# Kernel optimization log

Measured on AMD Instinct MI355X. Metric: run time of the kernel, lower is better.

The kernel has to match this reference:

```python
import jax, jax.numpy as jnp
from jax import lax
import numpy as np

B, T, C = 4, 1024, 1024
NH, HS = 16, 64
K, STRIDE = 32, 16
EPS = 1e-5


def _ln(x, w, b):
    m = jnp.mean(x, axis=-1, keepdims=True)
    v = jnp.mean((x - m) ** 2, axis=-1, keepdims=True)
    return (x - m) * lax.rsqrt(v + EPS) * w + b


def setup_inputs() -> dict:
    key = jax.random.key(0)
    ks = jax.random.split(key, 12)
    s = 0.02
    return {
        'x': jax.random.normal(ks[0], (B, T, C), jnp.float32),
        'c_attn_w': jax.random.normal(ks[1], (C, 3 * C), jnp.float32) * s,
        'c_attn_b': jnp.zeros((3 * C,), jnp.float32),
        'c_proj_w': jax.random.normal(ks[2], (C, C), jnp.float32) * s,
        'c_proj_b': jnp.zeros((C,), jnp.float32),
        'conv_w': jax.random.normal(ks[3], (HS, HS, K), jnp.float32) * s,  # OIH
        'conv_b': jnp.zeros((HS,), jnp.float32),
        'comp_ln_w': jnp.ones((HS,), jnp.float32),
        'comp_ln_b': jnp.zeros((HS,), jnp.float32),
        'ln_local_w': jnp.ones((C,), jnp.float32),
        'ln_local_b': jnp.zeros((C,), jnp.float32),
        'gate_w1': jax.random.normal(ks[4], (2 * C, C), jnp.float32) * s,
        'gate_b1': jnp.zeros((C,), jnp.float32),
        'gate_ln_w': jnp.ones((C,), jnp.float32),
        'gate_ln_b': jnp.zeros((C,), jnp.float32),
        'gate_w2': jax.random.normal(ks[5], (C, 2), jnp.float32) * s,
        'gate_b2': jnp.zeros((2,), jnp.float32),
    }


def _compress(h, conv_w, conv_b, comp_ln_w, comp_ln_b):
    # h: [B, nh, T, hs] -> [B, nh, num_blocks, hs]
    b, nh, t, hs = h.shape
    xr = h.transpose(0, 1, 3, 2).reshape(b * nh, hs, t)  # NCH
    co = lax.conv_general_dilated(xr, conv_w, (STRIDE,), 'VALID',
                                  dimension_numbers=('NCH', 'OIH', 'NCH'))
    co = co + conv_b[None, :, None]
    y = co.transpose(0, 2, 1)  # [B*nh, nb, hs]
    y = _ln(y, comp_ln_w, comp_ln_b)
    y = jax.nn.gelu(y, approximate=False)
    return y.reshape(b, nh, -1, hs)


def _attn(q, k, v, mask):
    # q:[B,nh,T,hs] k,v:[B,nh,Tk,hs], mask:[T,Tk] bool (True=keep)
    scale = 1.0 / jnp.sqrt(jnp.asarray(q.shape[-1], q.dtype))
    att = jnp.einsum('bhqd,bhkd->bhqk', q, k) * scale
    att = jnp.where(mask[None, None], att, jnp.finfo(att.dtype).min)
    att = jax.nn.softmax(att, axis=-1)
    return jnp.einsum('bhqk,bhkd->bhqd', att, v)


def reference(x, c_attn_w, c_attn_b, c_proj_w, c_proj_b, conv_w, conv_b,
              comp_ln_w, comp_ln_b, ln_local_w, ln_local_b,
              gate_w1, gate_b1, gate_ln_w, gate_ln_b, gate_w2, gate_b2):
    b, t, c = x.shape
    qkv = x @ c_attn_w + c_attn_b
    q, k, v = jnp.split(qkv, 3, axis=-1)
    q = q.reshape(b, t, NH, HS).transpose(0, 2, 1, 3)
    k = k.reshape(b, t, NH, HS).transpose(0, 2, 1, 3)
    v = v.reshape(b, t, NH, HS).transpose(0, 2, 1, 3)

    k_comp = _compress(k, conv_w, conv_b, comp_ln_w, comp_ln_b)
    v_comp = _compress(v, conv_w, conv_b, comp_ln_w, comp_ln_b)
    nb = k_comp.shape[2]

    # local branch: flash path with is_causal=True skips the window mask -> plain causal
    causal = jnp.tril(jnp.ones((t, t), bool))
    local = _attn(q, k, v, causal)
    local = local.transpose(0, 2, 1, 3).reshape(b, t, c)
    local_norm = _ln(local, ln_local_w, ln_local_b)

    # compressed branch: causal mask of shape [T, num_blocks], diagonal 0
    comp_mask = jnp.tril(jnp.ones((t, nb), bool), k=0)
    comp = _attn(q, k_comp, v_comp, comp_mask)
    comp = comp.transpose(0, 2, 1, 3).reshape(b, t, c)

    # gating from last-token features
    feats = jnp.concatenate([local_norm[:, -1, :], comp[:, -1, :]], axis=-1)  # [B, 2C]
    h = jax.nn.relu(_ln(feats @ gate_w1 + gate_b1, gate_ln_w, gate_ln_b))
    gates = jax.nn.softmax(h @ gate_w2 + gate_b2, axis=-1)  # [B, 2]
    g = gates[:, None, :]  # [B, 1, 2]
    combined = g[..., 0:1] * local_norm + g[..., 1:2] * comp

    return combined @ c_proj_w + c_proj_b
```

## Files before the change

### kernel.cpp

```cpp
#include <hip/hip_runtime.h>

using u16 = unsigned short;
using f32x4 = __attribute__((ext_vector_type(4))) float;
using s16x8 = __attribute__((ext_vector_type(8))) short;
using u16x4 = __attribute__((ext_vector_type(4))) unsigned short;

__device__ __forceinline__ u16 f2bf(float f) {
  unsigned u = __float_as_uint(f);
  return (u16)((u + 0x7FFFu + ((u >> 16) & 1u)) >> 16);
}

__device__ __forceinline__ f32x4 mfma16(s16x8 a, s16x8 b, f32x4 c) {
  return __builtin_amdgcn_mfma_f32_16x16x32_bf16(a, b, c, 0, 0, 0);
}

__device__ __forceinline__ void gld16(const void* g, void* l) {
  __builtin_amdgcn_global_load_lds(
      (const __attribute__((address_space(1))) unsigned int*)g,
      (__attribute__((address_space(3))) unsigned int*)l, 16, 0, 0);
}

__global__ __launch_bounds__(256) void cast_bf16(const float* __restrict__ in,
                                                 u16* __restrict__ out, int n4) {
  int i = blockIdx.x * 256 + threadIdx.x;
  if (i >= n4) return;
  f32x4 v = *(const f32x4*)(in + (size_t)i * 4);
  u16x4 o = {f2bf(v[0]), f2bf(v[1]), f2bf(v[2]), f2bf(v[3])};
  *(u16x4*)(out + (size_t)i * 4) = o;
}

__global__ __launch_bounds__(256) void transpose_cast(const float* __restrict__ in,
                                                      u16* __restrict__ out,
                                                      int R, int C) {
  __shared__ float t[32][33];
  int bx = blockIdx.x, by = blockIdx.y;
  int tx = threadIdx.x & 31, ty = threadIdx.x >> 5;
#pragma unroll
  for (int r = 0; r < 4; r++) {
    int row = by * 32 + ty + r * 8;
    t[ty + r * 8][tx] = in[(size_t)row * C + bx * 32 + tx];
  }
  __syncthreads();
#pragma unroll
  for (int r = 0; r < 4; r++) {
    int orow = bx * 32 + ty + r * 8;
    out[(size_t)orow * R + by * 32 + tx] = f2bf(t[tx][ty + r * 8]);
  }
}

__device__ __forceinline__ void gemm_mainloop(const u16* A, const u16* Bt, int K,
                                              u16* As, u16* Bs, f32x4 acc[4][4]) {
  const int tid = threadIdx.x;
  const int row = tid >> 2, c16 = tid & 3;
  const int lane = tid & 63, wid = tid >> 6;
  const int wm = wid >> 1, wn = wid & 1, lg = lane >> 4, lr = lane & 15;
  const u16* ga = A + (size_t)row * K + c16 * 8;
  const u16* gb = Bt + (size_t)row * K + c16 * 8;
  const size_t rowskip = (size_t)64 * K;
  for (int k0 = 0; k0 < K; k0 += 32) {
    gld16(ga + k0, As + tid * 8);
    gld16(ga + rowskip + k0, As + 2048 + tid * 8);
    gld16(gb + k0, Bs + tid * 8);
    gld16(gb + rowskip + k0, Bs + 2048 + tid * 8);
    __syncthreads();
    s16x8 af[4], bfr[4];
#pragma unroll
    for (int i = 0; i < 4; i++)
      af[i] = *(const s16x8*)(As + (wm * 64 + i * 16 + lr) * 32 + lg * 8);
#pragma unroll
    for (int j = 0; j < 4; j++)
      bfr[j] = *(const s16x8*)(Bs + (wn * 64 + j * 16 + lr) * 32 + lg * 8);
#pragma unroll
    for (int i = 0; i < 4; i++)
#pragma unroll
      for (int j = 0; j < 4; j++) acc[i][j] = mfma16(af[i], bfr[j], acc[i][j]);
    __syncthreads();
  }
}

__global__ __launch_bounds__(256) void gemm_qkv(const u16* __restrict__ A,
                                                const u16* __restrict__ Bt,
                                                const float* __restrict__ bias,
                                                u16* __restrict__ qo, u16* __restrict__ ko,
                                                u16* __restrict__ kTo, u16* __restrict__ vTo) {
  __shared__ u16 As[4096];
  __shared__ u16 Bs[4096];
  int m0 = blockIdx.x * 128, n0 = blockIdx.y * 128;
  f32x4 acc[4][4] = {};
  gemm_mainloop(A + (size_t)m0 * 1024, Bt + (size_t)n0 * 1024, 1024, As, Bs, acc);
  int lane = threadIdx.x & 63, wid = threadIdx.x >> 6;
  int wm = wid >> 1, wn = wid & 1, lg = lane >> 4, lr = lane & 15;
#pragma unroll
  for (int i = 0; i < 4; i++) {
    int mb = m0 + wm * 64 + i * 16 + lg * 4;
    int b = mb >> 10, tb = mb & 1023;
#pragma unroll
    for (int j = 0; j < 4; j++) {
      int n = n0 + wn * 64 + j * 16 + lr;
      float bs = bias[n];
      int sel = n >> 10, hd = n & 1023, h = hd >> 6, d = hd & 63;
      int bh = b * 16 + h;
      u16 u0 = f2bf(acc[i][j][0] + bs), u1 = f2bf(acc[i][j][1] + bs);
      u16 u2 = f2bf(acc[i][j][2] + bs), u3 = f2bf(acc[i][j][3] + bs);
      if (sel == 0) {
        u16* qp = qo + ((size_t)bh << 16) + ((size_t)tb << 6) + d;
        qp[0] = u0; qp[64] = u1; qp[128] = u2; qp[192] = u3;
      } else if (sel == 1) {
        u16* kp = ko + ((size_t)bh << 16) + ((size_t)tb << 6) + d;
        kp[0] = u0; kp[64] = u1; kp[128] = u2; kp[192] = u3;
        u16x4 pk = {u0, u1, u2, u3};
        *(u16x4*)(kTo + ((size_t)(bh * 64 + d) << 10) + tb) = pk;
      } else {
        u16x4 pk = {u0, u1, u2, u3};
        *(u16x4*)(vTo + ((size_t)(bh * 64 + d) << 10) + tb) = pk;
      }
    }
  }
}

__global__ __launch_bounds__(256) void gemm_proj(const u16* __restrict__ A,
                                                 const u16* __restrict__ Bt,
                                                 const float* __restrict__ bias,
                                                 float* __restrict__ out) {
  __shared__ u16 As[4096];
  __shared__ u16 Bs[4096];
  int m0 = blockIdx.x * 128, n0 = blockIdx.y * 128;
  f32x4 acc[4][4] = {};
  gemm_mainloop(A + (size_t)m0 * 1024, Bt + (size_t)n0 * 1024, 1024, As, Bs, acc);
  int lane = threadIdx.x & 63, wid = threadIdx.x >> 6;
  int wm = wid >> 1, wn = wid & 1, lg = lane >> 4, lr = lane & 15;
#pragma unroll
  for (int i = 0; i < 4; i++) {
    int mb = m0 + wm * 64 + i * 16 + lg * 4;
#pragma unroll
    for (int j = 0; j < 4; j++) {
      int n = n0 + wn * 64 + j * 16 + lr;
      float bs = bias[n];
#pragma unroll
      for (int r = 0; r < 4; r++)
        out[(size_t)(mb + r) * 1024 + n] = acc[i][j][r] + bs;
    }
  }
}

__global__ __launch_bounds__(256) void conv_comp(const u16* __restrict__ kT,
                                                 const u16* __restrict__ vT,
                                                 const u16* __restrict__ cw,
                                                 const float* __restrict__ cb,
                                                 const float* __restrict__ lnw,
                                                 const float* __restrict__ lnb,
                                                 u16* __restrict__ kcomp,
                                                 u16* __restrict__ vcompT) {
  int bh = blockIdx.x, sel = blockIdx.y;
  const u16* src = (sel ? vT : kT) + ((size_t)bh << 16);
  int tid = threadIdx.x, wid = tid >> 6, lane = tid & 63, lg = lane >> 4, lr = lane & 15;
  f32x4 acc[4] = {};
  int arow = wid * 16 + lr;
  if (arow > 62) arow = 62;
  const u16* abase = src + (size_t)arow * 16 + lg * 8;
#pragma unroll 4
  for (int ic = 0; ic < 64; ic++) {
    s16x8 a = *(const s16x8*)(abase + ic * 1024);
#pragma unroll
    for (int j = 0; j < 4; j++) {
      s16x8 bfr = *(const s16x8*)(cw + (size_t)(j * 16 + lr) * 2048 + ic * 32 + lg * 8);
      acc[j] = mfma16(a, bfr, acc[j]);
    }
  }
  float lwv[4], lbv[4];
#pragma unroll
  for (int j = 0; j < 4; j++) {
    int oc = j * 16 + lr;
    float cbv = cb[oc];
    acc[j][0] += cbv; acc[j][1] += cbv; acc[j][2] += cbv; acc[j][3] += cbv;
    lwv[j] = lnw[oc]; lbv[j] = lnb[oc];
  }
#pragma unroll
  for (int r = 0; r < 4; r++) {
    float s = acc[0][r] + acc[1][r] + acc[2][r] + acc[3][r];
    float q = acc[0][r] * acc[0][r] + acc[1][r] * acc[1][r] +
              acc[2][r] * acc[2][r] + acc[3][r] * acc[3][r];
#pragma unroll
    for (int off = 1; off < 16; off <<= 1) {
      s += __shfl_xor(s, off);
      q += __shfl_xor(q, off);
    }
    float mean = s * (1.f / 64.f);
    float var = q * (1.f / 64.f) - mean * mean;
    float rstd = rsqrtf(fmaxf(var, 0.f) + 1e-5f);
    int op = wid * 16 + lg * 4 + r;
#pragma unroll
    for (int j = 0; j < 4; j++) {
      float y = (acc[j][r] - mean) * rstd * lwv[j] + lbv[j];
      y = 0.5f * y * (1.0f + erff(y * 0.70710678118f));
      if (op > 62) y = 0.f;
      int oc = j * 16 + lr;
      if (sel == 0) kcomp[((size_t)bh << 12) + (op << 6) + oc] = f2bf(y);
      else          vcompT[((size_t)bh << 12) + (oc << 6) + op] = f2bf(y);
    }
  }
}

__global__ __launch_bounds__(256, 4) void flash64(const u16* __restrict__ qg,
                                                  const u16* __restrict__ kg,
                                                  const u16* __restrict__ vg,
                                                  float* __restrict__ outg,
                                                  int k_bh, int v_bh, int vrow, int kvmax) {
  __shared__ u16 Ks[2][4096];
  __shared__ u16 Pl[4][1152];
  const int tid = threadIdx.x;
  const int w = tid >> 6, lane = tid & 63, lg = lane >> 4, lr = lane & 15;
  const int idx = blockIdx.x;
  const int nqt = gridDim.x >> 6;
  const int xcd = idx & 7, j = idx >> 3;
  const int bh = xcd * 8 + (j & 7);
  const int qt0 = nqt - 1 - (j >> 3);
  const int q0 = qt0 * 64;
  const int qrow = q0 + w * 16 + lr;
  const u16* qb = qg + ((size_t)bh << 16) + (size_t)qrow * 64 + lg * 8;
  s16x8 qf0 = *(const s16x8*)(qb);
  s16x8 qf1 = *(const s16x8*)(qb + 32);
  const u16* kb = kg + (size_t)bh * k_bh;
  const u16* vb = vg + (size_t)bh * v_bh;
  int nt = qt0 + 1;
  int ntk = (kvmax + 63) >> 6;
  if (nt > ntk) nt = ntk;
  u16* Pw = Pl[w];
  f32x4 ot[4] = {};
  float m = -INFINITY, l = 0.f;
  const float SCL = 0.125f * 1.44269504089f;

  auto stageK = [&](int bufi, int kv0) {
#pragma unroll
    for (int rnd = 0; rnd < 2; rnd++) {
      int o = tid * 16 + rnd * 4096;
      int row = o >> 7;
      int sb = (o & 127) ^ ((row & 7) << 4);
      gld16(kb + (size_t)(kv0 + row) * 64 + (sb >> 1), &Ks[bufi][o >> 1]);
    }
  };

  stageK(0, 0);
  int cur = 0;
  for (int t = 0; t < nt; t++) {
    __syncthreads();
    if (t + 1 < nt) stageK(cur ^ 1, (t + 1) * 64);
    const int kv0 = t * 64;
    const u16* Kb = Ks[cur];
    const bool full = (kv0 + 63 <= q0 + w * 16) && (kv0 + 64 <= kvmax);
    s16x8 vlo[4];
#pragma unroll
    for (int d4 = 0; d4 < 4; d4++)
      vlo[d4] = *(const s16x8*)(vb + (size_t)(d4 * 16 + lr) * vrow + kv0 + lg * 8);
    f32x4 st[4];
    __builtin_amdgcn_s_setprio(1);
#pragma unroll
    for (int kvt = 0; kvt < 4; kvt++) {
      int rr = kvt * 16 + lr;
      int sw = (rr & 7) << 4;
      s16x8 k0 = *(const s16x8*)(Kb + (((rr << 7) + ((lg * 16) ^ sw)) >> 1));
      s16x8 k1 = *(const s16x8*)(Kb + (((rr << 7) + ((64 + lg * 16) ^ sw)) >> 1));
      f32x4 z = {};
      z = mfma16(k0, qf0, z);
      z = mfma16(k1, qf1, z);
      st[kvt] = z;
    }
    __builtin_amdgcn_s_setprio(0);
    s16x8 vhi[4];
#pragma unroll
    for (int d4 = 0; d4 < 4; d4++)
      vhi[d4] = *(const s16x8*)(vb + (size_t)(d4 * 16 + lr) * vrow + kv0 + 32 + lg * 8);
    float p[16];
    float tm = -INFINITY;
    if (full) {
#pragma unroll
      for (int kvt = 0; kvt < 4; kvt++)
#pragma unroll
        for (int r = 0; r < 4; r++) {
          float v = st[kvt][r] * SCL;
          p[kvt * 4 + r] = v;
          tm = fmaxf(tm, v);
        }
    } else {
#pragma unroll
      for (int kvt = 0; kvt < 4; kvt++)
#pragma unroll
        for (int r = 0; r < 4; r++) {
          int kvi = kv0 + kvt * 16 + lg * 4 + r;
          float v = st[kvt][r] * SCL;
          v = (kvi <= qrow && kvi < kvmax) ? v : -INFINITY;
          p[kvt * 4 + r] = v;
          tm = fmaxf(tm, v);
        }
    }
    tm = fmaxf(tm, __shfl_xor(tm, 16));
    tm = fmaxf(tm, __shfl_xor(tm, 32));
    if (!__all(tm <= m)) {
      float mnew = fmaxf(m, tm);
      float fac = exp2f(m - mnew);
      l *= fac;
#pragma unroll
      for (int d4 = 0; d4 < 4; d4++) {
        ot[d4][0] *= fac; ot[d4][1] *= fac; ot[d4][2] *= fac; ot[d4][3] *= fac;
      }
      m = mnew;
    }
    float ls = 0.f;
#pragma unroll
    for (int i = 0; i < 16; i++) {
      float e = exp2f(p[i] - m);
      p[i] = e;
      ls += e;
    }
    ls += __shfl_xor(ls, 16);
    ls += __shfl_xor(ls, 32);
    l += ls;
#pragma unroll
    for (int kvt = 0; kvt < 4; kvt++) {
      unsigned w0 = (unsigned)f2bf(p[kvt * 4 + 0]) | ((unsigned)f2bf(p[kvt * 4 + 1]) << 16);
      unsigned w1 = (unsigned)f2bf(p[kvt * 4 + 2]) | ((unsigned)f2bf(p[kvt * 4 + 3]) << 16);
      uint2 pk = {w0, w1};
      *(uint2*)(Pw + lr * 72 + kvt * 16 + lg * 4) = pk;
    }
    s16x8 bp0 = *(const s16x8*)(Pw + lr * 72 + lg * 8);
    s16x8 bp1 = *(const s16x8*)(Pw + lr * 72 + 32 + lg * 8);
    __builtin_amdgcn_s_setprio(1);
#pragma unroll
    for (int d4 = 0; d4 < 4; d4++) {
      ot[d4] = mfma16(vlo[d4], bp0, ot[d4]);
      ot[d4] = mfma16(vhi[d4], bp1, ot[d4]);
    }
    __builtin_amdgcn_s_setprio(0);
    cur ^= 1;
  }
  float inv = 1.f / l;
  int b = bh >> 4, h = bh & 15;
  float* op = outg + ((size_t)((b << 10) + qrow) << 10) + h * 64;
#pragma unroll
  for (int d4 = 0; d4 < 4; d4++) {
    f32x4 v;
#pragma unroll
    for (int c = 0; c < 4; c++) v[c] = ot[d4][c] * inv;
    *(f32x4*)(op + d4 * 16 + lg * 4) = v;
  }
}

__global__ __launch_bounds__(256) void ln_rows(float* __restrict__ x,
                                               const float* __restrict__ w,
                                               const float* __restrict__ b) {
  __shared__ float red[8];
  size_t row = blockIdx.x;
  float* xr = x + (row << 10);
  int tid = threadIdx.x;
  f32x4 v = *(const f32x4*)(xr + tid * 4);
  float s = v[0] + v[1] + v[2] + v[3];
  float q = v[0] * v[0] + v[1] * v[1] + v[2] * v[2] + v[3] * v[3];
#pragma unroll
  for (int off = 32; off >= 1; off >>= 1) {
    s += __shfl_xor(s, off);
    q += __shfl_xor(q, off);
  }
  int wid = tid >> 6;
  if ((tid & 63) == 0) { red[wid * 2] = s; red[wid * 2 + 1] = q; }
  __syncthreads();
  s = red[0] + red[2] + red[4] + red[6];
  q = red[1] + red[3] + red[5] + red[7];
  float mean = s * (1.0f / 1024.0f);
  float var = q * (1.0f / 1024.0f) - mean * mean;
  float rstd = rsqrtf(fmaxf(var, 0.f) + 1e-5f);
  f32x4 wv = *(const f32x4*)(w + tid * 4);
  f32x4 bv = *(const f32x4*)(b + tid * 4);
  f32x4 o;
#pragma unroll
  for (int c = 0; c < 4; c++) o[c] = (v[c] - mean) * rstd * wv[c] + bv[c];
  *(f32x4*)(xr + tid * 4) = o;
}

__global__ __launch_bounds__(256) void gate_partial(const float* __restrict__ ln,
                                                    const float* __restrict__ comp,
                                                    const float* __restrict__ w1,
                                                    float* __restrict__ partial) {
  __shared__ float f[4][32];
  int ib = blockIdx.x, i0 = ib * 32, tid = threadIdx.x;
  if (tid < 128) {
    int bb = tid >> 5, ii = tid & 31;
    int i = i0 + ii;
    const float* src = (i < 1024) ? ln : comp;
    int ic = i & 1023;
    f[bb][ii] = src[((size_t)(bb * 1024 + 1023) << 10) + ic];
  }
  __syncthreads();
  float acc[4][4] = {};
  for (int ii = 0; ii < 32; ii++) {
    float f0 = f[0][ii], f1 = f[1][ii], f2 = f[2][ii], f3 = f[3][ii];
#pragma unroll
    for (int jj = 0; jj < 4; jj++) {
      float w = w1[(size_t)(i0 + ii) * 1024 + jj * 256 + tid];
      acc[jj][0] += f0 * w; acc[jj][1] += f1 * w;
      acc[jj][2] += f2 * w; acc[jj][3] += f3 * w;
    }
  }
#pragma unroll
  for (int jj = 0; jj < 4; jj++)
#pragma unroll
    for (int bb = 0; bb < 4; bb++)
      partial[(size_t)((ib << 2) + bb) * 1024 + jj * 256 + tid] = acc[jj][bb];
}

__global__ __launch_bounds__(1024) void gate_finish(const float* __restrict__ partial,
                                                    const float* __restrict__ b1,
                                                    const float* __restrict__ lnw,
                                                    const float* __restrict__ lnb,
                                                    const float* __restrict__ w2,
                                                    const float* __restrict__ b2,
                                                    float* __restrict__ g) {
  __shared__ float redA[16], redB[16];
  int b = blockIdx.x, j = threadIdx.x;
  float s = b1[j];
#pragma unroll 4
  for (int ib = 0; ib < 64; ib++) s += partial[(size_t)((ib << 2) + b) * 1024 + j];
  float sa = s, sb = s * s;
#pragma unroll
  for (int off = 32; off >= 1; off >>= 1) {
    sa += __shfl_xor(sa, off);
    sb += __shfl_xor(sb, off);
  }
  int wid = j >> 6;
  if ((j & 63) == 0) { redA[wid] = sa; redB[wid] = sb; }
  __syncthreads();
  if (j == 0) {
    float A = 0, Bv = 0;
    for (int k2 = 0; k2 < 16; k2++) { A += redA[k2]; Bv += redB[k2]; }
    redA[0] = A; redB[0] = Bv;
  }
  __syncthreads();
  float S = redA[0], Q = redB[0];
  float mean = S * (1.f / 1024.f), var = Q * (1.f / 1024.f) - mean * mean;
  float rstd = rsqrtf(fmaxf(var, 0.f) + 1e-5f);
  float hn = (s - mean) * rstd * lnw[j] + lnb[j];
  hn = fmaxf(hn, 0.f);
  float c0 = hn * w2[j * 2], c1 = hn * w2[j * 2 + 1];
  __syncthreads();
  float ra = c0, rb = c1;
#pragma unroll
  for (int off = 32; off >= 1; off >>= 1) {
    ra += __shfl_xor(ra, off);
    rb += __shfl_xor(rb, off);
  }
  if ((j & 63) == 0) { redA[wid] = ra; redB[wid] = rb; }
  __syncthreads();
  if (j == 0) {
    float A = 0, Bv = 0;
    for (int k2 = 0; k2 < 16; k2++) { A += redA[k2]; Bv += redB[k2]; }
    A += b2[0]; Bv += b2[1];
    float mx = fmaxf(A, Bv);
    float e0 = __expf(A - mx), e1 = __expf(Bv - mx);
    float inv = 1.f / (e0 + e1);
    g[b * 2] = e0 * inv;
    g[b * 2 + 1] = e1 * inv;
  }
}

__global__ __launch_bounds__(256) void combine_k(const float* __restrict__ ln,
                                                 const float* __restrict__ comp,
                                                 const float* __restrict__ g,
                                                 u16* __restrict__ out) {
  size_t i = (size_t)blockIdx.x * 256 + threadIdx.x;
  size_t off = i << 2;
  int b = (int)(off >> 20);
  float g0 = g[b * 2], g1 = g[b * 2 + 1];
  f32x4 a = *(const f32x4*)(ln + off);
  f32x4 c = *(const f32x4*)(comp + off);
  u16x4 o = {f2bf(g0 * a[0] + g1 * c[0]), f2bf(g0 * a[1] + g1 * c[1]),
             f2bf(g0 * a[2] + g1 * c[2]), f2bf(g0 * a[3] + g1 * c[3])};
  *(u16x4*)(out + off) = o;
}

extern "C" void kernel_launch(void* const* d_in, const int* in_sizes, int n_in,
                              void* d_out, int out_size, void* d_ws, size_t ws_size,
                              hipStream_t stream) {
  const float* x        = (const float*)d_in[0];
  const float* c_attn_w = (const float*)d_in[1];
  const float* c_attn_b = (const float*)d_in[2];
  const float* c_proj_w = (const float*)d_in[3];
  const float* c_proj_b = (const float*)d_in[4];
  const float* conv_w   = (const float*)d_in[5];
  const float* conv_b   = (const float*)d_in[6];
  const float* comp_ln_w= (const float*)d_in[7];
  const float* comp_ln_b= (const float*)d_in[8];
  const float* ln_loc_w = (const float*)d_in[9];
  const float* ln_loc_b = (const float*)d_in[10];
  const float* gate_w1  = (const float*)d_in[11];
  const float* gate_b1  = (const float*)d_in[12];
  const float* gate_ln_w= (const float*)d_in[13];
  const float* gate_ln_b= (const float*)d_in[14];
  const float* gate_w2  = (const float*)d_in[15];
  const float* gate_b2  = (const float*)d_in[16];
  float* out = (float*)d_out;

  char* ws = (char*)d_ws;
  size_t off = 0;
  auto alloc = [&](size_t bytes) -> char* {
    char* p = ws + off;
    off += (bytes + 255) & ~(size_t)255;
    return p;
  };
  u16* x_bf     = (u16*)alloc(8388608);
  u16* attn_wT  = (u16*)alloc(6291456);
  u16* proj_wT  = (u16*)alloc(2097152);
  u16* conv_wbf = (u16*)alloc(262144);
  u16* q_bf     = (u16*)alloc(8388608);
  u16* k_bf     = (u16*)alloc(8388608);
  u16* kT_bf    = (u16*)alloc(8388608);
  u16* vT_bf    = (u16*)alloc(8388608);
  u16* k_comp   = (u16*)alloc(524288);
  u16* v_compT  = (u16*)alloc(524288);
  float* local  = (float*)alloc(16777216);
  float* comp   = (float*)alloc(16777216);
  float* partial= (float*)alloc(1048576);
  float* gbuf   = (float*)alloc(256);
  u16* combined = x_bf;
  if (off > ws_size) return;

  cast_bf16<<<dim3(4096), dim3(256), 0, stream>>>(x, x_bf, 1048576);
  transpose_cast<<<dim3(96, 32), dim3(256), 0, stream>>>(c_attn_w, attn_wT, 1024, 3072);
  transpose_cast<<<dim3(32, 32), dim3(256), 0, stream>>>(c_proj_w, proj_wT, 1024, 1024);
  cast_bf16<<<dim3(128), dim3(256), 0, stream>>>(conv_w, conv_wbf, 32768);

  gemm_qkv<<<dim3(32, 24), dim3(256), 0, stream>>>(x_bf, attn_wT, c_attn_b,
                                                   q_bf, k_bf, kT_bf, vT_bf);

  conv_comp<<<dim3(64, 2), dim3(256), 0, stream>>>(kT_bf, vT_bf, conv_wbf, conv_b,
                                                   comp_ln_w, comp_ln_b, k_comp, v_compT);

  flash64<<<dim3(1024), dim3(256), 0, stream>>>(q_bf, k_bf, vT_bf, local,
                                                65536, 65536, 1024, 1024);
  flash64<<<dim3(1024), dim3(256), 0, stream>>>(q_bf, k_comp, v_compT, comp,
                                                4096, 4096, 64, 63);

  ln_rows<<<dim3(4096), dim3(256), 0, stream>>>(local, ln_loc_w, ln_loc_b);

  gate_partial<<<dim3(64), dim3(256), 0, stream>>>(local, comp, gate_w1, partial);
  gate_finish<<<dim3(4), dim3(1024), 0, stream>>>(partial, gate_b1, gate_ln_w,
                                                  gate_ln_b, gate_w2, gate_b2, gbuf);

  combine_k<<<dim3(4096), dim3(256), 0, stream>>>(local, comp, gbuf, combined);
  gemm_proj<<<dim3(32, 8), dim3(256), 0, stream>>>(combined, proj_wT, c_proj_b, out);
}
```

Baseline: 301.6 us.

## Split conv reduction across two wave groups and prepack conv weights into MFMA fragments

Result: faster. 279.6 us (-7.3%).

```diff
diff --git a/kernel.cpp b/kernel.cpp
--- a/kernel.cpp
+++ b/kernel.cpp
@@ -27,6 +27,22 @@
   f32x4 v = *(const f32x4*)(in + (size_t)i * 4);
   u16x4 o = {f2bf(v[0]), f2bf(v[1]), f2bf(v[2]), f2bf(v[3])};
   *(u16x4*)(out + (size_t)i * 4) = o;
+}
+
+__global__ __launch_bounds__(256) void cast_wfrag(const float* __restrict__ in,
+                                                  u16* __restrict__ out) {
+  int t = blockIdx.x * 256 + threadIdx.x;
+  int c = t & 63, blk = t >> 6;
+  int j = blk & 3, ic = blk >> 2;
+  int lr = c >> 2, lg = c & 3;
+  const float* src = in + (size_t)(j * 16 + lr) * 2048 + ic * 32 + lg * 8;
+  f32x4 a = *(const f32x4*)(src);
+  f32x4 b = *(const f32x4*)(src + 4);
+  u16* dst = out + (size_t)t * 8;
+  u16x4 o0 = {f2bf(a[0]), f2bf(a[1]), f2bf(a[2]), f2bf(a[3])};
+  u16x4 o1 = {f2bf(b[0]), f2bf(b[1]), f2bf(b[2]), f2bf(b[3])};
+  *(u16x4*)(dst) = o0;
+  *(u16x4*)(dst + 4) = o1;
 }
 
 __global__ __launch_bounds__(256) void transpose_cast(const float* __restrict__ in,
@@ -143,30 +159,47 @@
   }
 }
 
-__global__ __launch_bounds__(256) void conv_comp(const u16* __restrict__ kT,
-                                                 const u16* __restrict__ vT,
-                                                 const u16* __restrict__ cw,
-                                                 const float* __restrict__ cb,
-                                                 const float* __restrict__ lnw,
-                                                 const float* __restrict__ lnb,
-                                                 u16* __restrict__ kcomp,
-                                                 u16* __restrict__ vcompT) {
+__global__ __launch_bounds__(512, 2) void conv_comp(const u16* __restrict__ kT,
+                                                    const u16* __restrict__ vT,
+                                                    const u16* __restrict__ wfrag,
+                                                    const float* __restrict__ cb,
+                                                    const float* __restrict__ lnw,
+                                                    const float* __restrict__ lnb,
+                                                    u16* __restrict__ kcomp,
+                                                    u16* __restrict__ vcompT) {
+  __shared__ float red[4][64][16];
   int bh = blockIdx.x, sel = blockIdx.y;
   const u16* src = (sel ? vT : kT) + ((size_t)bh << 16);
-  int tid = threadIdx.x, wid = tid >> 6, lane = tid & 63, lg = lane >> 4, lr = lane & 15;
+  int tid = threadIdx.x, w = tid >> 6, lane = tid & 63, lg = lane >> 4, lr = lane & 15;
+  int wq = w & 3, ichalf = w >> 2;
   f32x4 acc[4] = {};
-  int arow = wid * 16 + lr;
+  int arow = wq * 16 + lr;
   if (arow > 62) arow = 62;
   const u16* abase = src + (size_t)arow * 16 + lg * 8;
-#pragma unroll 4
-  for (int ic = 0; ic < 64; ic++) {
+  const u16* wbase = wfrag + (size_t)(lr * 4 + lg) * 8;
+  int ic0 = ichalf * 32;
+#pragma unroll 8
+  for (int ic = ic0; ic < ic0 + 32; ic++) {
     s16x8 a = *(const s16x8*)(abase + ic * 1024);
+    const u16* wrow = wbase + (size_t)ic * 2048;
 #pragma unroll
     for (int j = 0; j < 4; j++) {
-      s16x8 bfr = *(const s16x8*)(cw + (size_t)(j * 16 + lr) * 2048 + ic * 32 + lg * 8);
+      s16x8 bfr = *(const s16x8*)(wrow + j * 512);
       acc[j] = mfma16(a, bfr, acc[j]);
     }
   }
+  if (w >= 4) {
+#pragma unroll
+    for (int j = 0; j < 4; j++)
+#pragma unroll
+      for (int r = 0; r < 4; r++) red[wq][lane][j * 4 + r] = acc[j][r];
+  }
+  __syncthreads();
+  if (w >= 4) return;
+#pragma unroll
+  for (int j = 0; j < 4; j++)
+#pragma unroll
+    for (int r = 0; r < 4; r++) acc[j][r] += red[wq][lane][j * 4 + r];
   float lwv[4], lbv[4];
 #pragma unroll
   for (int j = 0; j < 4; j++) {
@@ -188,7 +221,7 @@
     float mean = s * (1.f / 64.f);
     float var = q * (1.f / 64.f) - mean * mean;
     float rstd = rsqrtf(fmaxf(var, 0.f) + 1e-5f);
-    int op = wid * 16 + lg * 4 + r;
+    int op = wq * 16 + lg * 4 + r;
 #pragma unroll
     for (int j = 0; j < 4; j++) {
       float y = (acc[j][r] - mean) * rstd * lwv[j] + lbv[j];
@@ -508,7 +541,7 @@
   u16* x_bf     = (u16*)alloc(8388608);
   u16* attn_wT  = (u16*)alloc(6291456);
   u16* proj_wT  = (u16*)alloc(2097152);
-  u16* conv_wbf = (u16*)alloc(262144);
+  u16* wfrag    = (u16*)alloc(262144);
   u16* q_bf     = (u16*)alloc(8388608);
   u16* k_bf     = (u16*)alloc(8388608);
   u16* kT_bf    = (u16*)alloc(8388608);
@@ -525,12 +558,12 @@
   cast_bf16<<<dim3(4096), dim3(256), 0, stream>>>(x, x_bf, 1048576);
   transpose_cast<<<dim3(96, 32), dim3(256), 0, stream>>>(c_attn_w, attn_wT, 1024, 3072);
   transpose_cast<<<dim3(32, 32), dim3(256), 0, stream>>>(c_proj_w, proj_wT, 1024, 1024);
-  cast_bf16<<<dim3(128), dim3(256), 0, stream>>>(conv_w, conv_wbf, 32768);
+  cast_wfrag<<<dim3(64), dim3(256), 0, stream>>>(conv_w, wfrag);
 
   gemm_qkv<<<dim3(32, 24), dim3(256), 0, stream>>>(x_bf, attn_wT, c_attn_b,
                                                    q_bf, k_bf, kT_bf, vT_bf);
 
-  conv_comp<<<dim3(64, 2), dim3(256), 0, stream>>>(kT_bf, vT_bf, conv_wbf, conv_b,
+  conv_comp<<<dim3(64, 2), dim3(512), 0, stream>>>(kT_bf, vT_bf, wfrag, conv_b,
                                                    comp_ln_w, comp_ln_b, k_comp, v_compT);
 
   flash64<<<dim3(1024), dim3(256), 0, stream>>>(q_bf, k_bf, vT_bf, local,
```
